# Performance work log

Measured on AMD Instinct MI355X. Metric: run time of the kernel, lower is better.

Reference implementation:

```python
import jax, jax.numpy as jnp
import numpy as np
from jax import lax

RES = 7
SCALE = 1.0 / 16.0


def _Fk(t):
    # antiderivative of the triangular bilinear kernel k(t)=max(0,1-|t|),
    # evaluated as integral from -1 to t (clamped to kernel support)
    t = jnp.clip(t, -1.0, 1.0)
    return jnp.where(t < 0, 0.5 * (t + 1.0) ** 2, 1.0 - 0.5 * (1.0 - t) ** 2)


def _bin_weights(lo, hi, L):
    # lo, hi: [R] roi start/end (feature coords). Returns ([R, RES, L], [R])
    bw = (hi - lo) / RES
    starts = lo[:, None] + bw[:, None] * jnp.arange(RES, dtype=lo.dtype)  # [R,RES]
    ends = starts + bw[:, None]
    idx = jnp.arange(L, dtype=lo.dtype)  # pixel centers
    # exact integral of bilinear kernel centered at each pixel over each bin
    W = _Fk(ends[:, :, None] - idx) - _Fk(starts[:, :, None] - idx)  # [R,RES,L]
    return W, bw


def prroi_pool(feat, bbox):
    # Precise RoI pooling: exact integral of bilinearly-interpolated feature
    # over each bin, which is separable in y and x.
    B, C, H, Wf = feat.shape
    R = bbox.shape[0]
    n = R // B  # boxes per frame (rois are grouped per frame, as in torch code)
    x1 = bbox[:, 0] * SCALE
    y1 = bbox[:, 1] * SCALE
    x2 = (bbox[:, 0] + bbox[:, 2]) * SCALE  # bbox stores (x1,y1,w,h)
    y2 = (bbox[:, 1] + bbox[:, 3]) * SCALE
    Wx, bwx = _bin_weights(x1, x2, Wf)
    Wy, bwy = _bin_weights(y1, y2, H)
    Wx = Wx.reshape(B, n, RES, Wf)
    Wy = Wy.reshape(B, n, RES, H)
    pooled = jnp.einsum('bnph,bchw,bnqw->bncpq', Wy, feat, Wx)  # [B,n,C,7,7]
    area = (bwx * bwy).reshape(B, n)[:, :, None, None, None]
    pooled = jnp.where(area > 0, pooled / jnp.maximum(area, 1e-12), 0.0)
    return pooled.reshape(R, C, RES, RES)


def _conv(x, w, pad):
    return lax.conv_general_dilated(x, w, (1, 1), ((pad, pad), (pad, pad)),
                                    dimension_numbers=('NCHW', 'OIHW', 'NCHW'))


def _cbn(x, w, s, b, pad):
    # conv (no bias) + FrozenBatchNorm (per-channel affine)
    return _conv(x, w, pad) * s[:, None, None] + b[:, None, None]


def _deconv2x2(x, w):
    # PyTorch ConvTranspose2d(k=2, s=2, p=0); w: [Cin, Cout, 2, 2]
    wc = jnp.flip(w, (2, 3)).transpose(1, 0, 2, 3)  # -> [Cout, Cin, 2, 2]
    return lax.conv_general_dilated(x, wc, (1, 1), ((1, 1), (1, 1)),
                                    lhs_dilation=(2, 2),
                                    dimension_numbers=('NCHW', 'OIHW', 'NCHW'))


def setup_inputs() -> dict:
    key = jax.random.key(0)
    ks = jax.random.split(key, 20)
    B, C, H, W = 16, 256, 36, 36
    R = 512  # 32 boxes per frame
    nb, bc = 3, 128
    g = 0.05
    feat = jax.random.normal(ks[0], (B, C, H, W), jnp.float32)
    u = jax.random.uniform(ks[1], (R, 4), jnp.float32)
    # (x1, y1, w, h) in image coords for a 576x576 search region
    bbox = jnp.concatenate([u[:, :2] * 400.0, 32.0 + u[:, 2:] * 128.0], axis=1)
    w1 = jax.random.normal(ks[2], (nb, bc, C, 1, 1), jnp.float32) * g
    s1 = jax.random.uniform(ks[3], (nb, bc), jnp.float32) * 0.5 + 0.5
    b1 = jax.random.normal(ks[4], (nb, bc), jnp.float32) * g
    w2 = jax.random.normal(ks[5], (nb, bc, bc, 3, 3), jnp.float32) * g
    s2 = jax.random.uniform(ks[6], (nb, bc), jnp.float32) * 0.5 + 0.5
    b2 = jax.random.normal(ks[7], (nb, bc), jnp.float32) * g
    w3 = jax.random.normal(ks[8], (nb, C, bc, 1, 1), jnp.float32) * g
    s3 = jax.random.uniform(ks[9], (nb, C), jnp.float32) * 0.5 + 0.5
    b3 = jax.random.normal(ks[10], (nb, C), jnp.float32) * g
    wt = jax.random.normal(ks[11], (C, 256, 2, 2), jnp.float32) * g
    bt = jax.random.normal(ks[12], (256,), jnp.float32) * g
    wm = jax.random.normal(ks[13], (1, 256, 1, 1), jnp.float32) * g
    bm = jax.random.normal(ks[14], (1,), jnp.float32) * g
    return dict(feat=feat, bbox=bbox, w1=w1, s1=s1, b1=b1, w2=w2, s2=s2, b2=b2,
                w3=w3, s3=s3, b3=b3, wt=wt, bt=bt, wm=wm, bm=bm)


def reference(feat, bbox, w1, s1, b1, w2, s2, b2, w3, s3, b3, wt, bt, wm, bm):
    x = prroi_pool(feat, bbox)  # [R, 256, 7, 7]
    # 3 bottleneck blocks with frozen BN (stride 1, no downsample: in==out)
    for i in range(w1.shape[0]):
        out = jax.nn.relu(_cbn(x, w1[i], s1[i], b1[i], 0))
        out = jax.nn.relu(_cbn(out, w2[i], s2[i], b2[i], 1))
        out = _cbn(out, w3[i], s3[i], b3[i], 0)
        x = jax.nn.relu(out + x)
    x = jax.nn.relu(_deconv2x2(x, wt) + bt[:, None, None])  # [R, 256, 14, 14]
    logits = _conv(x, wm, 0) + bm[:, None, None]  # [R, 1, 14, 14]
    return jax.nn.sigmoid(logits)  # eval-mode output
```

## Files before the change

kernel.cpp:

```cpp
#include <hip/hip_runtime.h>
#include <math.h>

#define RESQ 7
#define CH   256
#define NROI 512
#define BC   128
#define NB   3
#define NT   512

typedef __bf16 bh8  __attribute__((ext_vector_type(8)));
typedef float  f16v __attribute__((ext_vector_type(16)));

#define BAR() do { \
    asm volatile("s_waitcnt lgkmcnt(0)" ::: "memory"); \
    __builtin_amdgcn_s_barrier(); \
    asm volatile("" ::: "memory"); \
} while (0)

#define A1OFF 0
#define A2OFF 196608
#define A3OFF 1081344
#define ATOFF 1277952
#define WS_BYTES 1802240
#define FTOFF 1802240
#define WS_FULL 12419072
#define PRE_ELEMS 901120

#define XS_OFF 0
#define T1_OFF 25088
#define T2_OFF 45824
#define WY_OFF 58368
#define WX_OFF 59376
#define LG_OFF 60384
#define LDS_BYTES 64480

#define SWZ(row) (((row) & 15) << 4)

__device__ __forceinline__ float Fk(float t) {
    t = fminf(1.f, fmaxf(-1.f, t));
    float a = t + 1.f, b = 1.f - t;
    return (t < 0.f) ? 0.5f * a * a : 1.f - 0.5f * b * b;
}
__device__ __forceinline__ unsigned short bf16bits(float a) {
    return __builtin_bit_cast(unsigned short, (__bf16)a);
}
__device__ __forceinline__ unsigned int pk2(float a, float b) {
    return (unsigned int)bf16bits(a) | ((unsigned int)bf16bits(b) << 16);
}
__device__ __forceinline__ float b2f(unsigned int s) {
    return __builtin_bit_cast(float, s << 16);
}
__device__ __forceinline__ bh8 ld_bh8(const unsigned char* p) { return *(const bh8*)p; }
__device__ __forceinline__ bh8 cvt8(const float* p) {
    float4 a = *(const float4*)p;
    float4 b = *(const float4*)(p + 4);
    bh8 r;
    r[0]=(__bf16)a.x; r[1]=(__bf16)a.y; r[2]=(__bf16)a.z; r[3]=(__bf16)a.w;
    r[4]=(__bf16)b.x; r[5]=(__bf16)b.y; r[6]=(__bf16)b.z; r[7]=(__bf16)b.w;
    return r;
}
__device__ __forceinline__ bh8 gather8(const float* p, int stride) {
    bh8 r;
    #pragma unroll
    for (int j = 0; j < 8; ++j) r[j] = (__bf16)p[j * stride];
    return r;
}

__device__ __forceinline__ void epi_store(const f16v acc, int chbase, int h,
        const float* sarr, const float* barr, unsigned char* rowbase, int rswz) {
    #pragma unroll
    for (int g = 0; g < 4; ++g) {
        const int ch = chbase + 8*g + 4*h;
        const float4 sv = *(const float4*)(sarr + ch);
        const float4 bv = *(const float4*)(barr + ch);
        float v0 = fmaxf(fmaf(acc[4*g+0], sv.x, bv.x), 0.f);
        float v1 = fmaxf(fmaf(acc[4*g+1], sv.y, bv.y), 0.f);
        float v2 = fmaxf(fmaf(acc[4*g+2], sv.z, bv.z), 0.f);
        float v3 = fmaxf(fmaf(acc[4*g+3], sv.w, bv.w), 0.f);
        *(uint2*)(rowbase + ((2*ch) ^ rswz)) = make_uint2(pk2(v0,v1), pk2(v2,v3));
    }
}
__device__ __forceinline__ void epi_res(const f16v acc, int chbase, int h,
        const float* sarr, const float* barr, unsigned char* rowbase, int rswz) {
    #pragma unroll
    for (int g = 0; g < 4; ++g) {
        const int ch = chbase + 8*g + 4*h;
        const float4 sv = *(const float4*)(sarr + ch);
        const float4 bv = *(const float4*)(barr + ch);
        unsigned char* p = rowbase + ((2*ch) ^ rswz);
        const uint2 old = *(const uint2*)p;
        float v0 = fmaxf(fmaf(acc[4*g+0], sv.x, bv.x) + b2f(old.x & 0xFFFFu), 0.f);
        float v1 = fmaxf(fmaf(acc[4*g+1], sv.y, bv.y) + b2f(old.x >> 16), 0.f);
        float v2 = fmaxf(fmaf(acc[4*g+2], sv.z, bv.z) + b2f(old.y & 0xFFFFu), 0.f);
        float v3 = fmaxf(fmaf(acc[4*g+3], sv.w, bv.w) + b2f(old.y >> 16), 0.f);
        *(uint2*)p = make_uint2(pk2(v0,v1), pk2(v2,v3));
    }
}
__device__ __forceinline__ float dq_part(const f16v acc, int chbase, int h,
        const float* bt, const float* wm) {
    float part = 0.f;
    #pragma unroll
    for (int g = 0; g < 4; ++g) {
        const int ch = chbase + 8*g + 4*h;
        const float4 btv = *(const float4*)(bt + ch);
        const float4 wmv = *(const float4*)(wm + ch);
        part = fmaf(wmv.x, fmaxf(acc[4*g+0] + btv.x, 0.f), part);
        part = fmaf(wmv.y, fmaxf(acc[4*g+1] + btv.y, 0.f), part);
        part = fmaf(wmv.z, fmaxf(acc[4*g+2] + btv.z, 0.f), part);
        part = fmaf(wmv.w, fmaxf(acc[4*g+3] + btv.w, 0.f), part);
    }
    return part;
}

extern "C" __global__ void prep_all(const float* __restrict__ feat,
                                    const float* __restrict__ w1,
                                    const float* __restrict__ w2,
                                    const float* __restrict__ w3,
                                    const float* __restrict__ wt,
                                    unsigned char* __restrict__ ws,
                                    int do_ft) {
    __shared__ unsigned short tile[36 * 256];
    if (do_ft && blockIdx.x < 576) {
        const int b = blockIdx.x / 36, y = blockIdx.x % 36;
        const int c = threadIdx.x;
        const float* src = feat + (size_t)(b * 256 + c) * 1296 + y * 36;
        float4 fv[9];
        #pragma unroll
        for (int i = 0; i < 9; ++i) fv[i] = *(const float4*)(src + i * 4);
        #pragma unroll
        for (int i = 0; i < 9; ++i) {
            tile[(i*4+0)*256 + c] = bf16bits(fv[i].x);
            tile[(i*4+1)*256 + c] = bf16bits(fv[i].y);
            tile[(i*4+2)*256 + c] = bf16bits(fv[i].z);
            tile[(i*4+3)*256 + c] = bf16bits(fv[i].w);
        }
        __syncthreads();
        unsigned short* dst = (unsigned short*)(ws + FTOFF) + (size_t)(b*36 + y)*36*256;
        for (int x = 0; x < 36; ++x) dst[x*256 + c] = tile[x*256 + c];
        return;
    }
    const int base = do_ft ? 576 : 0;
    const int nb = gridDim.x - base;
    __bf16* wb = (__bf16*)ws;
    for (int i = (blockIdx.x - base) * blockDim.x + threadIdx.x; i < PRE_ELEMS;
         i += nb * blockDim.x) {
        float v; int dst;
        if (i < 98304) {
            int e = i;
            int j = e & 7, lane = (e>>3)&63, t = (e>>9)&15, mt = (e>>13)&3, ib = e>>15;
            int m = mt*32 + (lane&31), k = t*16 + 8*(lane>>5) + j;
            v = w1[(ib*BC + m)*CH + k];
            dst = (A1OFF>>1) + e;
        } else if (i < 98304 + 442368) {
            int e = i - 98304;
            int j = e & 7, lane = (e>>3)&63, t = (e>>9)&7, mt = (e>>12)&3;
            int rem = e >> 14;
            int ib = rem / 9, tap = rem - ib*9;
            int m = mt*32 + (lane&31), ci = t*16 + 8*(lane>>5) + j;
            v = w2[((ib*BC + m)*BC + ci)*9 + tap];
            dst = (A2OFF>>1) + e;
        } else if (i < 98304 + 442368 + 98304) {
            int e = i - (98304 + 442368);
            int j = e & 7, lane = (e>>3)&63, t = (e>>9)&7, mt = (e>>12)&7, ib = e>>15;
            int m = mt*32 + (lane&31), ci = t*16 + 8*(lane>>5) + j;
            v = w3[(ib*CH + m)*BC + ci];
            dst = (A3OFF>>1) + e;
        } else {
            int e = i - (98304 + 442368 + 98304);
            int j = e & 7, lane = (e>>3)&63, t = (e>>9)&15, mt = (e>>13)&7, quad = e>>16;
            int co = mt*32 + (lane&31), ci = t*16 + 8*(lane>>5) + j;
            v = wt[ci*1024 + co*4 + quad];
            dst = (ATOFF>>1) + e;
        }
        wb[dst] = (__bf16)v;
    }
}

template<int USE_WS, int USE_FT>
__global__ __launch_bounds__(NT, 2)
void masknet_mfma(const float* __restrict__ feat,
                  const float* __restrict__ bbox,
                  const float* __restrict__ w1, const float* __restrict__ s1, const float* __restrict__ b1,
                  const float* __restrict__ w2, const float* __restrict__ s2, const float* __restrict__ b2,
                  const float* __restrict__ w3, const float* __restrict__ s3, const float* __restrict__ b3,
                  const float* __restrict__ wt, const float* __restrict__ bt,
                  const float* __restrict__ wm, const float* __restrict__ bm,
                  const unsigned char* __restrict__ ws,
                  float* __restrict__ out)
{
    __shared__ __align__(16) unsigned char smem[LDS_BYTES];
    float* wyb = (float*)(smem + WY_OFF);
    float* wxb = (float*)(smem + WX_OFF);
    float* lgf = (float*)(smem + LG_OFF);

    const int tid  = threadIdx.x;
    const int r    = blockIdx.x;
    const int bfr  = r >> 5;
    const int lane = tid & 63;
    const int ln   = lane & 31;
    const int h    = lane >> 5;
    const int w_   = tid >> 6;
    const int cb   = 16 * h;

    const float S = 1.f / 16.f;
    const float bx = bbox[r*4+0], by = bbox[r*4+1];
    const float bw_ = bbox[r*4+2], bh_ = bbox[r*4+3];
    const float x1 = bx * S, y1 = by * S;
    const float bwx = (bw_ * S) * (1.f / RESQ);
    const float bwy = (bh_ * S) * (1.f / RESQ);
    const float area = bwx * bwy;
    const float inv_area = (area > 0.f) ? 1.f / fmaxf(area, 1e-12f) : 0.f;

    if (tid < 252) {
        int p = tid / 36, i = tid - p * 36;
        float st = y1 + bwy * p, en = st + bwy;
        wyb[tid] = Fk(en - (float)i) - Fk(st - (float)i);
    } else if (tid >= 256 && tid < 508) {
        int t = tid - 256;
        int q = t / 36, i = t - q * 36;
        float st = x1 + bwx * q, en = st + bwx;
        wxb[t] = Fk(en - (float)i) - Fk(st - (float)i);
    }
    {
        uint4* z = (uint4*)(smem + T1_OFF);
        for (int o = tid; o < 1296; o += NT) z[o] = make_uint4(0,0,0,0);
        for (int o = tid; o < 1024; o += NT) lgf[o] = 0.f;
    }
    BAR();

    if (USE_FT) {
        const unsigned short* ft = (const unsigned short*)(ws + FTOFF) + (size_t)bfr * (1296 * 256);
        const int g = w_ * 2 + h;
        #pragma unroll 1
        for (int k = 0; k < 4; ++k) {
            const int s = g + 16 * k;
            if (s >= 49) break;
            const int p = s / 7, q = s - p * 7;
            const float sy = y1 + bwy * p, sx = x1 + bwx * q;
            const int ylo = max(0, (int)floorf(sy)), yhi = min(35, (int)ceilf(sy + bwy));
            const int xlo = max(0, (int)floorf(sx)), xhi = min(35, (int)ceilf(sx + bwx));
            float wyv[4], wxv[4];
            #pragma unroll
            for (int j = 0; j < 4; ++j) {
                const int y = ylo + j, x = xlo + j;
                wyv[j] = (y <= yhi) ? wyb[p*36 + y] * inv_area : 0.f;
                wxv[j] = (x <= xhi) ? wxb[q*36 + x] : 0.f;
            }
            float ac0=0.f,ac1=0.f,ac2=0.f,ac3=0.f,ac4=0.f,ac5=0.f,ac6=0.f,ac7=0.f;
            #pragma unroll
            for (int yy = 0; yy < 4; ++yy) {
                const int y = min(ylo + yy, 35);
                const unsigned short* rowp = ft + (size_t)(y * 36) * 256 + ln * 8;
                #pragma unroll
                for (int xx = 0; xx < 4; ++xx) {
                    const int x = min(xlo + xx, 35);
                    const float wgt = wyv[yy] * wxv[xx];
                    const uint4 v = *(const uint4*)(rowp + x * 256);
                    ac0 = fmaf(wgt, b2f(v.x & 0xFFFFu), ac0);
                    ac1 = fmaf(wgt, b2f(v.x >> 16),     ac1);
                    ac2 = fmaf(wgt, b2f(v.y & 0xFFFFu), ac2);
                    ac3 = fmaf(wgt, b2f(v.y >> 16),     ac3);
                    ac4 = fmaf(wgt, b2f(v.z & 0xFFFFu), ac4);
                    ac5 = fmaf(wgt, b2f(v.z >> 16),     ac5);
                    ac6 = fmaf(wgt, b2f(v.w & 0xFFFFu), ac6);
                    ac7 = fmaf(wgt, b2f(v.w >> 16),     ac7);
                }
            }
            *(uint4*)(smem + XS_OFF + s * 512 + ((16 * ln) ^ SWZ(s))) =
                make_uint4(pk2(ac0,ac1), pk2(ac2,ac3), pk2(ac4,ac5), pk2(ac6,ac7));
        }
    } else {
        const float* fb = feat + (size_t)bfr * CH * 36 * 36;
        for (int o = tid; o < CH * 49; o += NT) {
            int c = o / 49, s = o - c * 49;
            int p = s / 7, q = s - p * 7;
            float sy = y1 + bwy * p, sx = x1 + bwx * q;
            int ylo = max(0, (int)floorf(sy)), yhi = min(35, (int)ceilf(sy + bwy));
            int xlo = max(0, (int)floorf(sx)), xhi = min(35, (int)ceilf(sx + bwx));
            const float* fc = fb + c * 1296;
            float acc = 0.f;
            for (int y = ylo; y <= yhi; ++y) {
                float wyv = wyb[p * 36 + y];
                for (int x = xlo; x <= xhi; ++x)
                    acc = fmaf(wyv * wxb[q * 36 + x], fc[y * 36 + x], acc);
            }
            *(unsigned short*)(smem + XS_OFF + s * 512 + ((2 * c) ^ SWZ(s))) =
                bf16bits(acc * inv_area);
        }
    }

    const int mt12 = w_ & 3, nt12 = w_ >> 2;
    const int col12 = nt12 * 32 + ln;
    const int ncl12 = min(col12, 48);
    const int mg = w_ >> 1, ng = w_ & 1;
    const int col3 = ng * 32 + ln;
    const int ncl3 = min(col3, 48);

    bh8 pf[4] = {};
    if (USE_WS) {
        #pragma unroll
        for (int t = 0; t < 4; ++t)
            pf[t] = ld_bh8(ws + A1OFF + ((((0*4 + mt12)*16 + t)*64 + lane) << 4));
    }
    BAR();

    #pragma unroll 1
    for (int ib = 0; ib < NB; ++ib) {
        {
            const unsigned char* bb = smem + XS_OFF + ncl12 * 512;
            const int bswz = SWZ(ncl12);
            f16v acc = {};
            #pragma unroll
            for (int t = 0; t < 16; ++t) {
                bh8 a;
                if (USE_WS) a = (t < 4) ? pf[t]
                                        : ld_bh8(ws + A1OFF + ((((ib*4 + mt12)*16 + t)*64 + lane) << 4));
                else        a = cvt8(w1 + (size_t)(ib*BC + mt12*32 + ln)*CH + t*16 + 8*h);
                bh8 b = ld_bh8(bb + ((t*32 + cb) ^ bswz));
                acc = __builtin_amdgcn_mfma_f32_32x32x16_bf16(a, b, acc, 0, 0, 0);
            }
            if (col12 < 49) {
                const int row = (col12/7 + 1)*9 + (col12 - (col12/7)*7) + 1;
                epi_store(acc, mt12*32, h, s1 + ib*BC, b1 + ib*BC,
                          smem + T1_OFF + row*256, SWZ(row));
            }
        }
        if (USE_WS) {
            #pragma unroll
            for (int t = 0; t < 4; ++t)
                pf[t] = ld_bh8(ws + A2OFF + (((((ib*9+0)*4 + mt12)*8 + t)*64 + lane) << 4));
        }
        BAR();

        {
            const int tr0 = (ncl12/7)*9 + (ncl12 - (ncl12/7)*7);
            f16v acc = {};
            #pragma unroll 1
            for (int ty = 0; ty < 3; ++ty) {
                #pragma unroll
                for (int tx = 0; tx < 3; ++tx) {
                    const int tap = ty*3 + tx;
                    bh8 aw[8];
                    #pragma unroll
                    for (int t = 0; t < 8; ++t) {
                        if (USE_WS) aw[t] = (ty == 0 && tx == 0 && t < 4) ? pf[t]
                                          : ld_bh8(ws + A2OFF + (((((ib*9+tap)*4 + mt12)*8 + t)*64 + lane) << 4));
                        else        aw[t] = gather8(w2 + ((size_t)(ib*BC + mt12*32 + ln)*BC + t*16 + 8*h)*9 + tap, 9);
                    }
                    const int row = tr0 + ty*9 + tx;
                    const unsigned char* bb = smem + T1_OFF + row*256;
                    const int rs = SWZ(row);
                    #pragma unroll
                    for (int t = 0; t < 8; ++t) {
                        bh8 b = ld_bh8(bb + ((t*32 + cb) ^ rs));
                        acc = __builtin_amdgcn_mfma_f32_32x32x16_bf16(aw[t], b, acc, 0, 0, 0);
                    }
                }
            }
            if (col12 < 49) {
                epi_store(acc, mt12*32, h, s2 + ib*BC, b2 + ib*BC,
                          smem + T2_OFF + col12*256, SWZ(col12));
            }
        }
        if (USE_WS) {
            #pragma unroll
            for (int t = 0; t < 4; ++t)
                pf[t] = ld_bh8(ws + A3OFF + ((((ib*8 + 2*mg+0)*8 + t)*64 + lane) << 4));
        }
        BAR();

        {
            const unsigned char* bb = smem + T2_OFF + ncl3 * 256;
            const int bswz = SWZ(ncl3);
            f16v acc0 = {}, acc1 = {};
            #pragma unroll
            for (int t = 0; t < 8; ++t) {
                bh8 a0, a1;
                if (USE_WS) {
                    a0 = (t < 4) ? pf[t]
                                 : ld_bh8(ws + A3OFF + ((((ib*8 + 2*mg+0)*8 + t)*64 + lane) << 4));
                    a1 = ld_bh8(ws + A3OFF + ((((ib*8 + 2*mg+1)*8 + t)*64 + lane) << 4));
                } else {
                    a0 = cvt8(w3 + (size_t)(ib*CH + (2*mg+0)*32 + ln)*BC + t*16 + 8*h);
                    a1 = cvt8(w3 + (size_t)(ib*CH + (2*mg+1)*32 + ln)*BC + t*16 + 8*h);
                }
                bh8 b = ld_bh8(bb + ((t*32 + cb) ^ bswz));
                acc0 = __builtin_amdgcn_mfma_f32_32x32x16_bf16(a0, b, acc0, 0, 0, 0);
                acc1 = __builtin_amdgcn_mfma_f32_32x32x16_bf16(a1, b, acc1, 0, 0, 0);
            }
            if (col3 < 49) {
                unsigned char* rowb = smem + XS_OFF + col3*512;
                const int rs = SWZ(col3);
                epi_res(acc0, (2*mg+0)*32, h, s3 + ib*CH, b3 + ib*CH, rowb, rs);
                epi_res(acc1, (2*mg+1)*32, h, s3 + ib*CH, b3 + ib*CH, rowb, rs);
            }
        }
        if (USE_WS) {
            #pragma unroll
            for (int t = 0; t < 4; ++t) {
                if (ib < NB - 1)
                    pf[t] = ld_bh8(ws + A1OFF + (((((ib+1)*4 + mt12)*16 + t)*64 + lane) << 4));
                else
                    pf[t] = ld_bh8(ws + ATOFF + ((((0*8 + 2*mg+0)*16 + t)*64 + lane) << 4));
            }
        }
        BAR();
    }

    {
        const unsigned char* bb = smem + XS_OFF + ncl3 * 512;
        const int bswz = SWZ(ncl3);
        {
            f16v acc0 = {}, acc1 = {};
            #pragma unroll
            for (int t = 0; t < 16; ++t) {
                bh8 b = ld_bh8(bb + ((t*32 + cb) ^ bswz));
                bh8 a0, a1;
                if (USE_WS) {
                    a0 = (t < 4) ? pf[t]
                                 : ld_bh8(ws + ATOFF + ((((0*8 + 2*mg+0)*16 + t)*64 + lane) << 4));
                    a1 = ld_bh8(ws + ATOFF + ((((0*8 + 2*mg+1)*16 + t)*64 + lane) << 4));
                } else {
                    a0 = gather8(wt + (size_t)(t*16 + 8*h)*1024 + ((2*mg+0)*32 + ln)*4 + 0, 1024);
                    a1 = gather8(wt + (size_t)(t*16 + 8*h)*1024 + ((2*mg+1)*32 + ln)*4 + 0, 1024);
                }
                acc0 = __builtin_amdgcn_mfma_f32_32x32x16_bf16(a0, b, acc0, 0, 0, 0);
                acc1 = __builtin_amdgcn_mfma_f32_32x32x16_bf16(a1, b, acc1, 0, 0, 0);
            }
            float p0 = dq_part(acc0, (2*mg+0)*32, h, bt, wm)
                     + dq_part(acc1, (2*mg+1)*32, h, bt, wm);
            p0 += __shfl_down(p0, 32);
            if (h == 0 && col3 < 49) lgf[(0*4 + mg)*64 + col3] = p0;
        }
        #pragma unroll 1
        for (int quad = 1; quad < 4; ++quad) {
            f16v acc0 = {}, acc1 = {};
            #pragma unroll
            for (int t = 0; t < 16; ++t) {
                bh8 b = ld_bh8(bb + ((t*32 + cb) ^ bswz));
                bh8 a0, a1;
                if (USE_WS) {
                    a0 = ld_bh8(ws + ATOFF + ((((quad*8 + 2*mg+0)*16 + t)*64 + lane) << 4));
                    a1 = ld_bh8(ws + ATOFF + ((((quad*8 + 2*mg+1)*16 + t)*64 + lane) << 4));
                } else {
                    a0 = gather8(wt + (size_t)(t*16 + 8*h)*1024 + ((2*mg+0)*32 + ln)*4 + quad, 1024);
                    a1 = gather8(wt + (size_t)(t*16 + 8*h)*1024 + ((2*mg+1)*32 + ln)*4 + quad, 1024);
                }
                acc0 = __builtin_amdgcn_mfma_f32_32x32x16_bf16(a0, b, acc0, 0, 0, 0);
                acc1 = __builtin_amdgcn_mfma_f32_32x32x16_bf16(a1, b, acc1, 0, 0, 0);
            }
            float p0 = dq_part(acc0, (2*mg+0)*32, h, bt, wm)
                     + dq_part(acc1, (2*mg+1)*32, h, bt, wm);
            p0 += __shfl_down(p0, 32);
            if (h == 0 && col3 < 49) lgf[(quad*4 + mg)*64 + col3] = p0;
        }
    }
    BAR();

    if (tid < 196) {
        const int quad = tid / 49, s = tid - quad*49;
        const float val = lgf[(quad*4+0)*64 + s] + lgf[(quad*4+1)*64 + s]
                        + lgf[(quad*4+2)*64 + s] + lgf[(quad*4+3)*64 + s] + bm[0];
        const int p = s / 7, q = s - p*7;
        const int dy = quad >> 1, dx = quad & 1;
        out[(size_t)r * 196 + (2*p + dy)*14 + (2*q + dx)] = 1.f / (1.f + expf(-val));
    }
}

extern "C" void kernel_launch(void* const* d_in, const int* in_sizes, int n_in,
                              void* d_out, int out_size, void* d_ws, size_t ws_size,
                              hipStream_t stream) {
    const float* feat = (const float*)d_in[0];
    const float* bbox = (const float*)d_in[1];
    const float* w1   = (const float*)d_in[2];
    const float* s1   = (const float*)d_in[3];
    const float* b1   = (const float*)d_in[4];
    const float* w2   = (const float*)d_in[5];
    const float* s2   = (const float*)d_in[6];
    const float* b2   = (const float*)d_in[7];
    const float* w3   = (const float*)d_in[8];
    const float* s3   = (const float*)d_in[9];
    const float* b3   = (const float*)d_in[10];
    const float* wt   = (const float*)d_in[11];
    const float* bt   = (const float*)d_in[12];
    const float* wm   = (const float*)d_in[13];
    const float* bm   = (const float*)d_in[14];
    float* out = (float*)d_out;

    if (ws_size >= (size_t)WS_FULL) {
        unsigned char* ws = (unsigned char*)d_ws;
        hipLaunchKernelGGL(prep_all, dim3(1024), dim3(256), 0, stream,
                           feat, w1, w2, w3, wt, ws, 1);
        hipLaunchKernelGGL((masknet_mfma<1,1>), dim3(NROI), dim3(NT), 0, stream,
                           feat, bbox, w1, s1, b1, w2, s2, b2, w3, s3, b3,
                           wt, bt, wm, bm, ws, out);
    } else if (ws_size >= (size_t)WS_BYTES) {
        unsigned char* ws = (unsigned char*)d_ws;
        hipLaunchKernelGGL(prep_all, dim3(448), dim3(256), 0, stream,
                           feat, w1, w2, w3, wt, ws, 0);
        hipLaunchKernelGGL((masknet_mfma<1,0>), dim3(NROI), dim3(NT), 0, stream,
                           feat, bbox, w1, s1, b1, w2, s2, b2, w3, s3, b3,
                           wt, bt, wm, bm, ws, out);
    } else {
        hipLaunchKernelGGL((masknet_mfma<0,0>), dim3(NROI), dim3(NT), 0, stream,
                           feat, bbox, w1, s1, b1, w2, s2, b2, w3, s3, b3,
                           wt, bt, wm, bm, (const unsigned char*)nullptr, out);
    }
}
```

Before: 115.4 us.

## Halve block to four waves, each looping over both column tiles

```diff
diff --git a/kernel.cpp b/kernel.cpp
--- a/kernel.cpp
+++ b/kernel.cpp
@@ -6,7 +6,7 @@
 #define NROI 512
 #define BC   128
 #define NB   3
-#define NT   512
+#define NT   256
 
 typedef __bf16 bh8  __attribute__((ext_vector_type(8)));
 typedef float  f16v __attribute__((ext_vector_type(16)));
@@ -211,15 +211,17 @@
     const float area = bwx * bwy;
     const float inv_area = (area > 0.f) ? 1.f / fmaxf(area, 1e-12f) : 0.f;
 
-    if (tid < 252) {
-        int p = tid / 36, i = tid - p * 36;
-        float st = y1 + bwy * p, en = st + bwy;
-        wyb[tid] = Fk(en - (float)i) - Fk(st - (float)i);
-    } else if (tid >= 256 && tid < 508) {
-        int t = tid - 256;
-        int q = t / 36, i = t - q * 36;
-        float st = x1 + bwx * q, en = st + bwx;
-        wxb[t] = Fk(en - (float)i) - Fk(st - (float)i);
+    for (int t = tid; t < 504; t += NT) {
+        if (t < 252) {
+            int p = t / 36, i = t - p * 36;
+            float st = y1 + bwy * p, en = st + bwy;
+            wyb[t] = Fk(en - (float)i) - Fk(st - (float)i);
+        } else {
+            int u = t - 252;
+            int q = u / 36, i = u - q * 36;
+            float st = x1 + bwx * q, en = st + bwx;
+            wxb[u] = Fk(en - (float)i) - Fk(st - (float)i);
+        }
     }
     {
         uint4* z = (uint4*)(smem + T1_OFF);
@@ -232,8 +234,8 @@
         const unsigned short* ft = (const unsigned short*)(ws + FTOFF) + (size_t)bfr * (1296 * 256);
         const int g = w_ * 2 + h;
         #pragma unroll 1
-        for (int k = 0; k < 4; ++k) {
-            const int s = g + 16 * k;
+        for (int k = 0; k < 7; ++k) {
+            const int s = g + 8 * k;
             if (s >= 49) break;
             const int p = s / 7, q = s - p * 7;
             const float sy = y1 + bwy * p, sx = x1 + bwx * q;
@@ -289,51 +291,48 @@
         }
     }
 
-    const int mt12 = w_ & 3, nt12 = w_ >> 2;
-    const int col12 = nt12 * 32 + ln;
-    const int ncl12 = min(col12, 48);
-    const int mg = w_ >> 1, ng = w_ & 1;
-    const int col3 = ng * 32 + ln;
-    const int ncl3 = min(col3, 48);
-
     bh8 pf[4] = {};
     if (USE_WS) {
         #pragma unroll
         for (int t = 0; t < 4; ++t)
-            pf[t] = ld_bh8(ws + A1OFF + ((((0*4 + mt12)*16 + t)*64 + lane) << 4));
+            pf[t] = ld_bh8(ws + A1OFF + ((((0*4 + w_)*16 + t)*64 + lane) << 4));
     }
     BAR();
 
     #pragma unroll 1
     for (int ib = 0; ib < NB; ++ib) {
-        {
-            const unsigned char* bb = smem + XS_OFF + ncl12 * 512;
-            const int bswz = SWZ(ncl12);
+        #pragma unroll 1
+        for (int nt = 0; nt < 2; ++nt) {
+            const int col = nt*32 + ln, ncl = min(col, 48);
+            const unsigned char* bb = smem + XS_OFF + ncl * 512;
+            const int bswz = SWZ(ncl);
             f16v acc = {};
             #pragma unroll
             for (int t = 0; t < 16; ++t) {
                 bh8 a;
-                if (USE_WS) a = (t < 4) ? pf[t]
-                                        : ld_bh8(ws + A1OFF + ((((ib*4 + mt12)*16 + t)*64 + lane) << 4));
-                else        a = cvt8(w1 + (size_t)(ib*BC + mt12*32 + ln)*CH + t*16 + 8*h);
+                if (USE_WS) a = (nt == 0 && t < 4) ? pf[t]
+                                : ld_bh8(ws + A1OFF + ((((ib*4 + w_)*16 + t)*64 + lane) << 4));
+                else        a = cvt8(w1 + (size_t)(ib*BC + w_*32 + ln)*CH + t*16 + 8*h);
                 bh8 b = ld_bh8(bb + ((t*32 + cb) ^ bswz));
                 acc = __builtin_amdgcn_mfma_f32_32x32x16_bf16(a, b, acc, 0, 0, 0);
             }
-            if (col12 < 49) {
-                const int row = (col12/7 + 1)*9 + (col12 - (col12/7)*7) + 1;
-                epi_store(acc, mt12*32, h, s1 + ib*BC, b1 + ib*BC,
+            if (col < 49) {
+                const int row = (col/7 + 1)*9 + (col - (col/7)*7) + 1;
+                epi_store(acc, w_*32, h, s1 + ib*BC, b1 + ib*BC,
                           smem + T1_OFF + row*256, SWZ(row));
             }
         }
         if (USE_WS) {
             #pragma unroll
             for (int t = 0; t < 4; ++t)
-                pf[t] = ld_bh8(ws + A2OFF + (((((ib*9+0)*4 + mt12)*8 + t)*64 + lane) << 4));
+                pf[t] = ld_bh8(ws + A2OFF + (((((ib*9+0)*4 + w_)*8 + t)*64 + lane) << 4));
         }
         BAR();
 
-        {
-            const int tr0 = (ncl12/7)*9 + (ncl12 - (ncl12/7)*7);
+        #pragma unroll 1
+        for (int nt = 0; nt < 2; ++nt) {
+            const int col = nt*32 + ln, ncl = min(col, 48);
+            const int tr0 = (ncl/7)*9 + (ncl - (ncl/7)*7);
             f16v acc = {};
             #pragma unroll 1
             for (int ty = 0; ty < 3; ++ty) {
@@ -343,9 +342,9 @@
                     bh8 aw[8];
                     #pragma unroll
                     for (int t = 0; t < 8; ++t) {
-                        if (USE_WS) aw[t] = (ty == 0 && tx == 0 && t < 4) ? pf[t]
-                                          : ld_bh8(ws + A2OFF + (((((ib*9+tap)*4 + mt12)*8 + t)*64 + lane) << 4));
-                        else        aw[t] = gather8(w2 + ((size_t)(ib*BC + mt12*32 + ln)*BC + t*16 + 8*h)*9 + tap, 9);
+                        if (USE_WS) aw[t] = (nt == 0 && ty == 0 && tx == 0 && t < 4) ? pf[t]
+                                          : ld_bh8(ws + A2OFF + (((((ib*9+tap)*4 + w_)*8 + t)*64 + lane) << 4));
+                        else        aw[t] = gather8(w2 + ((size_t)(ib*BC + w_*32 + ln)*BC + t*16 + 8*h)*9 + tap, 9);
                     }
                     const int row = tr0 + ty*9 + tx;
                     const unsigned char* bb = smem + T1_OFF + row*256;
@@ -357,102 +356,85 @@
                     }
                 }
             }
-            if (col12 < 49) {
-                epi_store(acc, mt12*32, h, s2 + ib*BC, b2 + ib*BC,
-                          smem + T2_OFF + col12*256, SWZ(col12));
+            if (col < 49) {
+                epi_store(acc, w_*32, h, s2 + ib*BC, b2 + ib*BC,
+                          smem + T2_OFF + col*256, SWZ(col));
             }
         }
         if (USE_WS) {
             #pragma unroll
             for (int t = 0; t < 4; ++t)
-                pf[t] = ld_bh8(ws + A3OFF + ((((ib*8 + 2*mg+0)*8 + t)*64 + lane) << 4));
+                pf[t] = ld_bh8(ws + A3OFF + ((((ib*8 + 2*w_+0)*8 + t)*64 + lane) << 4));
         }
         BAR();
 
-        {
-            const unsigned char* bb = smem + T2_OFF + ncl3 * 256;
-            const int bswz = SWZ(ncl3);
+        #pragma unroll 1
+        for (int nt = 0; nt < 2; ++nt) {
+            const int col = nt*32 + ln, ncl = min(col, 48);
+            const unsigned char* bb = smem + T2_OFF + ncl * 256;
+            const int bswz = SWZ(ncl);
             f16v acc0 = {}, acc1 = {};
             #pragma unroll
             for (int t = 0; t < 8; ++t) {
                 bh8 a0, a1;
                 if (USE_WS) {
-                    a0 = (t < 4) ? pf[t]
-                                 : ld_bh8(ws + A3OFF + ((((ib*8 + 2*mg+0)*8 + t)*64 + lane) << 4));
-                    a1 = ld_bh8(ws + A3OFF + ((((ib*8 + 2*mg+1)*8 + t)*64 + lane) << 4));
+                    a0 = (nt == 0 && t < 4) ? pf[t]
+                                 : ld_bh8(ws + A3OFF + ((((ib*8 + 2*w_+0)*8 + t)*64 + lane) << 4));
+                    a1 = ld_bh8(ws + A3OFF + ((((ib*8 + 2*w_+1)*8 + t)*64 + lane) << 4));
                 } else {
-                    a0 = cvt8(w3 + (size_t)(ib*CH + (2*mg+0)*32 + ln)*BC + t*16 + 8*h);
-                    a1 = cvt8(w3 + (size_t)(ib*CH + (2*mg+1)*32 + ln)*BC + t*16 + 8*h);
+                    a0 = cvt8(w3 + (size_t)(ib*CH + (2*w_+0)*32 + ln)*BC + t*16 + 8*h);
+                    a1 = cvt8(w3 + (size_t)(ib*CH + (2*w_+1)*32 + ln)*BC + t*16 + 8*h);
                 }
                 bh8 b = ld_bh8(bb + ((t*32 + cb) ^ bswz));
                 acc0 = __builtin_amdgcn_mfma_f32_32x32x16_bf16(a0, b, acc0, 0, 0, 0);
                 acc1 = __builtin_amdgcn_mfma_f32_32x32x16_bf16(a1, b, acc1, 0, 0, 0);
             }
-            if (col3 < 49) {
-                unsigned char* rowb = smem + XS_OFF + col3*512;
-                const int rs = SWZ(col3);
-                epi_res(acc0, (2*mg+0)*32, h, s3 + ib*CH, b3 + ib*CH, rowb, rs);
-                epi_res(acc1, (2*mg+1)*32, h, s3 + ib*CH, b3 + ib*CH, rowb, rs);
+            if (col < 49) {
+                unsigned char* rowb = smem + XS_OFF + col*512;
+                const int rs = SWZ(col);
+                epi_res(acc0, (2*w_+0)*32, h, s3 + ib*CH, b3 + ib*CH, rowb, rs);
+                epi_res(acc1, (2*w_+1)*32, h, s3 + ib*CH, b3 + ib*CH, rowb, rs);
             }
         }
         if (USE_WS) {
             #pragma unroll
             for (int t = 0; t < 4; ++t) {
                 if (ib < NB - 1)
-                    pf[t] = ld_bh8(ws + A1OFF + (((((ib+1)*4 + mt12)*16 + t)*64 + lane) << 4));
+                    pf[t] = ld_bh8(ws + A1OFF + (((((ib+1)*4 + w_)*16 + t)*64 + lane) << 4));
                 else
-                    pf[t] = ld_bh8(ws + ATOFF + ((((0*8 + 2*mg+0)*16 + t)*64 + lane) << 4));
+                    pf[t] = ld_bh8(ws + ATOFF + ((((0*8 + 2*w_+0)*16 + t)*64 + lane) << 4));
             }
         }
         BAR();
     }
 
-    {
-        const unsigned char* bb = smem + XS_OFF + ncl3 * 512;
-        const int bswz = SWZ(ncl3);
-        {
+    #pragma unroll 1
+    for (int quad = 0; quad < 4; ++quad) {
+        #pragma unroll 1
+        for (int nt = 0; nt < 2; ++nt) {
+            const int col = nt*32 + ln, ncl = min(col, 48);
+            const unsigned char* bb = smem + XS_OFF + ncl * 512;
+            const int bswz = SWZ(ncl);
             f16v acc0 = {}, acc1 = {};
             #pragma unroll
             for (int t = 0; t < 16; ++t) {
                 bh8 b = ld_bh8(bb + ((t*32 + cb) ^ bswz));
                 bh8 a0, a1;
                 if (USE_WS) {
-                    a0 = (t < 4) ? pf[t]
-                                 : ld_bh8(ws + ATOFF + ((((0*8 + 2*mg+0)*16 + t)*64 + lane) << 4));
-                    a1 = ld_bh8(ws + ATOFF + ((((0*8 + 2*mg+1)*16 + t)*64 + lane) << 4));
+                    a0 = (quad == 0 && nt == 0 && t < 4) ? pf[t]
+                                 : ld_bh8(ws + ATOFF + ((((quad*8 + 2*w_+0)*16 + t)*64 + lane) << 4));
+                    a1 = ld_bh8(ws + ATOFF + ((((quad*8 + 2*w_+1)*16 + t)*64 + lane) << 4));
                 } else {
-                    a0 = gather8(wt + (size_t)(t*16 + 8*h)*1024 + ((2*mg+0)*32 + ln)*4 + 0, 1024);
-                    a1 = gather8(wt + (size_t)(t*16 + 8*h)*1024 + ((2*mg+1)*32 + ln)*4 + 0, 1024);
+                    a0 = gather8(wt + (size_t)(t*16 + 8*h)*1024 + ((2*w_+0)*32 + ln)*4 + quad, 1024);
+                    a1 = gather8(wt + (size_t)(t*16 + 8*h)*1024 + ((2*w_+1)*32 + ln)*4 + quad, 1024);
                 }
                 acc0 = __builtin_amdgcn_mfma_f32_32x32x16_bf16(a0, b, acc0, 0, 0, 0);
                 acc1 = __builtin_amdgcn_mfma_f32_32x32x16_bf16(a1, b, acc1, 0, 0, 0);
             }
-            float p0 = dq_part(acc0, (2*mg+0)*32, h, bt, wm)
-                     + dq_part(acc1, (2*mg+1)*32, h, bt, wm);
+            float p0 = dq_part(acc0, (2*w_+0)*32, h, bt, wm)
+                     + dq_part(acc1, (2*w_+1)*32, h, bt, wm);
             p0 += __shfl_down(p0, 32);
-            if (h == 0 && col3 < 49) lgf[(0*4 + mg)*64 + col3] = p0;
-        }
-        #pragma unroll 1
-        for (int quad = 1; quad < 4; ++quad) {
-            f16v acc0 = {}, acc1 = {};
-            #pragma unroll
-            for (int t = 0; t < 16; ++t) {
-                bh8 b = ld_bh8(bb + ((t*32 + cb) ^ bswz));
-                bh8 a0, a1;
-                if (USE_WS) {
-                    a0 = ld_bh8(ws + ATOFF + ((((quad*8 + 2*mg+0)*16 + t)*64 + lane) << 4));
-                    a1 = ld_bh8(ws + ATOFF + ((((quad*8 + 2*mg+1)*16 + t)*64 + lane) << 4));
-                } else {
-                    a0 = gather8(wt + (size_t)(t*16 + 8*h)*1024 + ((2*mg+0)*32 + ln)*4 + quad, 1024);
-                    a1 = gather8(wt + (size_t)(t*16 + 8*h)*1024 + ((2*mg+1)*32 + ln)*4 + quad, 1024);
-                }
-                acc0 = __builtin_amdgcn_mfma_f32_32x32x16_bf16(a0, b, acc0, 0, 0, 0);
-                acc1 = __builtin_amdgcn_mfma_f32_32x32x16_bf16(a1, b, acc1, 0, 0, 0);
-            }
-            float p0 = dq_part(acc0, (2*mg+0)*32, h, bt, wm)
-                     + dq_part(acc1, (2*mg+1)*32, h, bt, wm);
-            p0 += __shfl_down(p0, 32);
-            if (h == 0 && col3 < 49) lgf[(quad*4 + mg)*64 + col3] = p0;
+            if (h == 0 && col < 49) lgf[(quad*4 + w_)*64 + col] = p0;
         }
     }
     BAR();
```

New measurement: 119.8 us. +3.8%, slower.
